# Performance work log

Measured on AMD Instinct MI355X. Metric: run time of the kernel, lower is better.

## Reference

```python
import jax, jax.numpy as jnp
import numpy as np

N_NODES = 100000


def gcn_conv(x, edge_index, W, b, n_nodes):
    """PyG GCNConv: add self-loops, symmetric deg norm, linear, scatter-add, bias."""
    self_loops = jnp.arange(n_nodes, dtype=edge_index.dtype)
    src = jnp.concatenate([edge_index[0], self_loops])  # [E+N]
    dst = jnp.concatenate([edge_index[1], self_loops])  # [E+N]
    xw = x @ W  # [N, out]
    deg = jax.ops.segment_sum(jnp.ones_like(dst, dtype=xw.dtype), dst, num_segments=n_nodes)
    deg_inv_sqrt = jnp.where(deg > 0, jax.lax.rsqrt(deg), 0.0)
    norm = deg_inv_sqrt[src] * deg_inv_sqrt[dst]  # [E+N]
    msg = xw[src] * norm[:, None]                 # [E+N, out]
    out = jax.ops.segment_sum(msg, dst, num_segments=n_nodes)
    return out + b


def setup_inputs() -> dict:
    key = jax.random.key(0)
    ks = jax.random.split(key, 8)
    n, e, d_in, h = N_NODES, 3200000, 128, 16
    x = jax.random.normal(ks[0], (n, d_in), dtype=jnp.float32)
    edge_index = jax.random.randint(ks[1], (2, e), 0, n, dtype=jnp.int64)
    W1 = jax.random.normal(ks[2], (d_in, h), dtype=jnp.float32) / np.sqrt(d_in)
    b1 = jnp.zeros((h,), dtype=jnp.float32)
    W2 = jax.random.normal(ks[3], (h, h), dtype=jnp.float32) / np.sqrt(h)
    b2 = jnp.zeros((h,), dtype=jnp.float32)
    W_lin = jax.random.normal(ks[4], (h, 1), dtype=jnp.float32) / np.sqrt(h)
    b_lin = jnp.zeros((1,), dtype=jnp.float32)
    return {"x": x, "edge_index": edge_index, "W1": W1, "b1": b1,
            "W2": W2, "b2": b2, "W_lin": W_lin, "b_lin": b_lin}


def reference(x, edge_index, W1, b1, W2, b2, W_lin, b_lin):
    n = x.shape[0]
    h = gcn_conv(x, edge_index, W1, b1, n)
    h = jax.nn.relu(h)
    # dropout is identity in eval mode (training=False)
    h = gcn_conv(h, edge_index, W2, b2, n)
    h = jax.nn.relu(h)
    out = h @ W_lin + b_lin  # [N, 1]
    return out.squeeze(-1)   # [N]
```

## Files before the change

### kernel.cpp

```cpp
#include <hip/hip_runtime.h>
#include <hip/hip_fp16.h>

#define DIN 128
#define HDIM 16
#define NB 256
#define CAP 13312
#define CAPC 14848
#define CAPH (CAPC / 2)
#define BIN_EPT 16
#define BINSZ (256 * BIN_EPT)

__device__ __forceinline__ float4 f4add(float4 a, float4 b) {
    return make_float4(a.x + b.x, a.y + b.y, a.z + b.z, a.w + b.w);
}

__device__ __forceinline__ float4 h4_to_f4(uint2 u) {
    __half2 a = *(__half2*)&u.x, b = *(__half2*)&u.y;
    float2 fa = __half22float2(a), fb = __half22float2(b);
    return make_float4(fa.x, fa.y, fb.x, fb.y);
}
__device__ __forceinline__ uint2 f4_to_h4(float4 v) {
    __half2 a = __floats2half2_rn(v.x, v.y);
    __half2 b = __floats2half2_rn(v.z, v.w);
    uint2 u;
    u.x = *(unsigned*)&a;
    u.y = *(unsigned*)&b;
    return u;
}

__device__ __forceinline__ int load_idx(const void* ei, long long i, int is64) {
    return is64 ? (int)((const long long*)ei)[i] : ((const int*)ei)[i];
}

__global__ __launch_bounds__(256) void k_main(const void* __restrict__ ei, long long E,
                                              int bdiv, unsigned Mdiv,
                                              int* __restrict__ bcur,
                                              unsigned int* __restrict__ recs,
                                              const float* __restrict__ x,
                                              const float* __restrict__ W1,
                                              unsigned int* __restrict__ y1,
                                              int n, int nbin) {
    __shared__ int cnt[NB];
    __shared__ int base[NB];
    __shared__ float Ws[DIN * HDIM];
    int tid = threadIdx.x;
    if ((int)blockIdx.x < nbin) {
        unsigned probe = ((const unsigned*)ei)[1 + 2 * (tid & 63)];
        int is64 = (__ballot(probe != 0) == 0ull) ? 1 : 0;
        if (tid < NB) cnt[tid] = 0;
        __syncthreads();
        long long e0 = (long long)blockIdx.x * BINSZ;
        int s[BIN_EPT], dl[BIN_EPT], b[BIN_EPT];
#pragma unroll
        for (int i = 0; i < BIN_EPT; i++) {
            long long e = e0 + (long long)i * 256 + tid;
            if (e < E) {
                s[i] = load_idx(ei, e, is64);
                int d = load_idx(ei, E + e, is64);
                int bb = Mdiv ? (int)__umulhi((unsigned)d, Mdiv) : d;
                b[i] = bb;
                dl[i] = d - bb * bdiv;
                atomicAdd(&cnt[bb], 1);
            } else {
                b[i] = -1;
            }
        }
        __syncthreads();
        if (tid < NB) {
            base[tid] = atomicAdd(&bcur[tid], cnt[tid]);
            cnt[tid] = 0;
        }
        __syncthreads();
#pragma unroll
        for (int i = 0; i < BIN_EPT; i++) {
            if (b[i] >= 0) {
                int off = atomicAdd(&cnt[b[i]], 1);
                int pos = base[b[i]] + off;
                if (pos < CAP) {
                    recs[(size_t)b[i] * CAP + pos] =
                        ((unsigned)dl[i] << 18) | (unsigned)s[i];
                }
            }
        }
    } else {
        for (int i = tid; i < DIN * HDIM; i += 256) Ws[i] = W1[i];
        __syncthreads();
        int node = ((int)blockIdx.x - nbin) * 256 + tid;
        if (node > n) return;
        uint2* yr = (uint2*)(y1 + (size_t)node * 8);
        if (node == n) {
            uint2 z; z.x = 0u; z.y = 0u;
#pragma unroll
            for (int q = 0; q < 4; q++) yr[q] = z;
            return;
        }
        float acc[HDIM];
#pragma unroll
        for (int f = 0; f < HDIM; f++) acc[f] = 0.f;
        const float4* xr = (const float4*)(x + (size_t)node * DIN);
#pragma unroll 8
        for (int k4 = 0; k4 < DIN / 4; k4++) {
            float4 xv = xr[k4];
            int k = k4 * 4;
#pragma unroll
            for (int f = 0; f < HDIM; f++) {
                acc[f] += xv.x * Ws[(k + 0) * HDIM + f];
                acc[f] += xv.y * Ws[(k + 1) * HDIM + f];
                acc[f] += xv.z * Ws[(k + 2) * HDIM + f];
                acc[f] += xv.w * Ws[(k + 3) * HDIM + f];
            }
        }
#pragma unroll
        for (int q = 0; q < 4; q++)
            yr[q] = f4_to_h4(make_float4(acc[q * 4 + 0], acc[q * 4 + 1],
                                         acc[q * 4 + 2], acc[q * 4 + 3]));
    }
}

__global__ __launch_bounds__(512) void k_prep(const unsigned int* __restrict__ recs,
                                              const int* __restrict__ bcur,
                                              float* __restrict__ dis,
                                              unsigned int* __restrict__ meta,
                                              int* __restrict__ col,
                                              unsigned int* __restrict__ y1,
                                              int bdiv, int n) {
    __shared__ int cnt_sh[256];
    __shared__ int sc[256];
    __shared__ unsigned short buf[CAPH];
    int tid = threadIdx.x;
    int b = (int)blockIdx.x >> 1;
    int h = (int)blockIdx.x & 1;
    int hd = (bdiv + 1) >> 1;
    int lo_f = b * bdiv; if (lo_f > n) lo_f = n;
    int hi_f = lo_f + bdiv; if (hi_f > n) hi_f = n;
    int lo = lo_f + h * hd; if (lo > hi_f) lo = hi_f;
    int hi = lo + hd; if (hi > hi_f) hi = hi_f;
    int nd = hi - lo;
    int dbase = h * hd;
    if (tid < 256) cnt_sh[tid] = 0;
    __syncthreads();
    int m = bcur[b]; if (m > CAP) m = CAP;
    const unsigned int* r = recs + (size_t)b * CAP;
    for (int i = tid; i < m; i += 512) {
        int j = (int)(r[i] >> 18) - dbase;
        if ((unsigned)j < (unsigned)nd) atomicAdd(&cnt_sh[j], 1);
    }
    __syncthreads();
    int v  = (tid < nd) ? cnt_sh[tid] : 0;
    int pv = (v + 3) & ~3;
    if (tid < 256) sc[tid] = pv;
    __syncthreads();
    for (int off = 1; off < 256; off <<= 1) {
        int t = (tid >= off && tid < 256) ? sc[tid - off] : 0;
        __syncthreads();
        if (tid < 256) sc[tid] += t;
        __syncthreads();
    }
    int ptot = sc[255];
    if (ptot > CAPH) ptot = CAPH;
    int cbase = b * CAPC + h * CAPH;
    if (tid < nd) {
        int excl = sc[tid] - pv;
        dis[lo + tid] = rsqrtf((float)v + 1.0f);
        meta[lo + tid] = ((unsigned)(cbase + excl) << 10) | (unsigned)v;
        cnt_sh[tid] = excl;
    }
    for (int i = tid; i < ptot; i += 512) buf[i] = 0xFFFFu;
    __syncthreads();
    for (int i = tid; i < m; i += 512) {
        int j = (int)(r[i] >> 18) - dbase;
        if ((unsigned)j < (unsigned)nd) {
            int pos = atomicAdd(&cnt_sh[j], 1);
            if (pos < CAPH) buf[pos] = (unsigned short)i;
        }
    }
    __syncthreads();
    for (int i = tid; i < ptot; i += 512) {
        unsigned short bi = buf[i];
        col[cbase + i] = (bi == 0xFFFFu) ? n : (int)(r[bi] & 0x3FFFFu);
    }
    int q = tid & 3, slot = tid >> 2;
    uint2* yv = (uint2*)y1;
    for (int j = slot; j < nd; j += 128) {
        int node = lo + j;
        float dv = dis[node];
        float4 t = h4_to_f4(yv[(size_t)node * 4 + q]);
        yv[(size_t)node * 4 + q] =
            f4_to_h4(make_float4(t.x * dv, t.y * dv, t.z * dv, t.w * dv));
    }
}

__global__ __launch_bounds__(256) void k_gather1(const unsigned int* __restrict__ meta,
                                                 const int* __restrict__ col,
                                                 const unsigned int* __restrict__ y1,
                                                 const float* __restrict__ dis,
                                                 const float* __restrict__ b1,
                                                 const float* __restrict__ W2,
                                                 unsigned int* __restrict__ y2, int n) {
    __shared__ float4 Ws4[HDIM][4];
    if (threadIdx.x < HDIM * 4)
        ((float4*)Ws4)[threadIdx.x] = ((const float4*)W2)[threadIdx.x];
    __syncthreads();
    if (blockIdx.x == 0 && threadIdx.x < 4) {
        uint2 z; z.x = 0u; z.y = 0u;
        ((uint2*)y2)[(size_t)n * 4 + threadIdx.x] = z;
    }
    int ln = threadIdx.x >> 2;
    int q  = threadIdx.x & 3;
    int node = blockIdx.x * 64 + ln;
    if (node >= n) return;
    unsigned mt = meta[node];
    int start = (int)(mt >> 10);
    int endp  = start + (((int)(mt & 1023u) + 3) & ~3);
    const uint2* yv = (const uint2*)y1;
    float4 a0 = make_float4(0.f, 0.f, 0.f, 0.f), a1 = a0, a2 = a0, a3 = a0;
    int e = start;
    for (; e + 16 <= endp; e += 16) {
        int4 c4 = *(const int4*)(col + e + 4 * q);
        int s[16];
#pragma unroll
        for (int j = 0; j < 4; j++) {
            s[4 * j + 0] = __shfl(c4.x, j, 4);
            s[4 * j + 1] = __shfl(c4.y, j, 4);
            s[4 * j + 2] = __shfl(c4.z, j, 4);
            s[4 * j + 3] = __shfl(c4.w, j, 4);
        }
        uint2 v[16];
#pragma unroll
        for (int k = 0; k < 16; k++) v[k] = yv[(size_t)s[k] * 4 + q];
#pragma unroll
        for (int k = 0; k < 16; k += 4) {
            a0 = f4add(a0, h4_to_f4(v[k + 0]));
            a1 = f4add(a1, h4_to_f4(v[k + 1]));
            a2 = f4add(a2, h4_to_f4(v[k + 2]));
            a3 = f4add(a3, h4_to_f4(v[k + 3]));
        }
    }
    for (; e < endp; e += 4) {
        int4 c4 = *(const int4*)(col + e);
        uint2 v0 = yv[(size_t)c4.x * 4 + q];
        uint2 v1 = yv[(size_t)c4.y * 4 + q];
        uint2 v2 = yv[(size_t)c4.z * 4 + q];
        uint2 v3 = yv[(size_t)c4.w * 4 + q];
        a0 = f4add(a0, h4_to_f4(v0)); a1 = f4add(a1, h4_to_f4(v1));
        a2 = f4add(a2, h4_to_f4(v2)); a3 = f4add(a3, h4_to_f4(v3));
    }
    float4 acc = f4add(f4add(a0, a1), f4add(a2, a3));
    acc = f4add(acc, h4_to_f4(yv[(size_t)node * 4 + q]));
    float dv = dis[node];
    float4 bb = ((const float4*)b1)[q];
    float4 h;
    h.x = fmaxf(dv * acc.x + bb.x, 0.f);
    h.y = fmaxf(dv * acc.y + bb.y, 0.f);
    h.z = fmaxf(dv * acc.z + bb.z, 0.f);
    h.w = fmaxf(dv * acc.w + bb.w, 0.f);
    float4 o = make_float4(0.f, 0.f, 0.f, 0.f);
#pragma unroll
    for (int k = 0; k < 4; k++) {
        float4 hk;
        hk.x = __shfl(h.x, k, 4); hk.y = __shfl(h.y, k, 4);
        hk.z = __shfl(h.z, k, 4); hk.w = __shfl(h.w, k, 4);
        float hv[4] = {hk.x, hk.y, hk.z, hk.w};
#pragma unroll
        for (int c = 0; c < 4; c++) {
            float4 w = Ws4[k * 4 + c][q];
            o.x += hv[c] * w.x; o.y += hv[c] * w.y;
            o.z += hv[c] * w.z; o.w += hv[c] * w.w;
        }
    }
    ((uint2*)y2)[(size_t)node * 4 + q] =
        f4_to_h4(make_float4(o.x * dv, o.y * dv, o.z * dv, o.w * dv));
}

__global__ __launch_bounds__(256) void k_gather2(const unsigned int* __restrict__ meta,
                                                 const int* __restrict__ col,
                                                 const unsigned int* __restrict__ y2,
                                                 const float* __restrict__ dis,
                                                 const float* __restrict__ b2,
                                                 const float* __restrict__ Wlin,
                                                 const float* __restrict__ blin,
                                                 float* __restrict__ out, int n) {
    int ln = threadIdx.x >> 2;
    int q  = threadIdx.x & 3;
    int node = blockIdx.x * 64 + ln;
    if (node >= n) return;
    unsigned mt = meta[node];
    int start = (int)(mt >> 10);
    int endp  = start + (((int)(mt & 1023u) + 3) & ~3);
    const uint2* yv = (const uint2*)y2;
    float4 a0 = make_float4(0.f, 0.f, 0.f, 0.f), a1 = a0, a2 = a0, a3 = a0;
    int e = start;
    for (; e + 16 <= endp; e += 16) {
        int4 c4 = *(const int4*)(col + e + 4 * q);
        int s[16];
#pragma unroll
        for (int j = 0; j < 4; j++) {
            s[4 * j + 0] = __shfl(c4.x, j, 4);
            s[4 * j + 1] = __shfl(c4.y, j, 4);
            s[4 * j + 2] = __shfl(c4.z, j, 4);
            s[4 * j + 3] = __shfl(c4.w, j, 4);
        }
        uint2 v[16];
#pragma unroll
        for (int k = 0; k < 16; k++) v[k] = yv[(size_t)s[k] * 4 + q];
#pragma unroll
        for (int k = 0; k < 16; k += 4) {
            a0 = f4add(a0, h4_to_f4(v[k + 0]));
            a1 = f4add(a1, h4_to_f4(v[k + 1]));
            a2 = f4add(a2, h4_to_f4(v[k + 2]));
            a3 = f4add(a3, h4_to_f4(v[k + 3]));
        }
    }
    for (; e < endp; e += 4) {
        int4 c4 = *(const int4*)(col + e);
        uint2 v0 = yv[(size_t)c4.x * 4 + q];
        uint2 v1 = yv[(size_t)c4.y * 4 + q];
        uint2 v2 = yv[(size_t)c4.z * 4 + q];
        uint2 v3 = yv[(size_t)c4.w * 4 + q];
        a0 = f4add(a0, h4_to_f4(v0)); a1 = f4add(a1, h4_to_f4(v1));
        a2 = f4add(a2, h4_to_f4(v2)); a3 = f4add(a3, h4_to_f4(v3));
    }
    float4 acc = f4add(f4add(a0, a1), f4add(a2, a3));
    acc = f4add(acc, h4_to_f4(yv[(size_t)node * 4 + q]));
    float dv = dis[node];
    float4 bb = ((const float4*)b2)[q];
    float4 wl = ((const float4*)Wlin)[q];
    float v = 0.f;
    v += fmaxf(dv * acc.x + bb.x, 0.f) * wl.x;
    v += fmaxf(dv * acc.y + bb.y, 0.f) * wl.y;
    v += fmaxf(dv * acc.z + bb.z, 0.f) * wl.z;
    v += fmaxf(dv * acc.w + bb.w, 0.f) * wl.w;
    v += __shfl_xor(v, 1, 4);
    v += __shfl_xor(v, 2, 4);
    if (q == 0) out[node] = v + blin[0];
}

extern "C" void kernel_launch(void* const* d_in, const int* in_sizes, int n_in,
                              void* d_out, int out_size, void* d_ws, size_t ws_size,
                              hipStream_t stream) {
    const float* x    = (const float*)d_in[0];
    const void*  ei   = d_in[1];
    const float* W1   = (const float*)d_in[2];
    const float* b1   = (const float*)d_in[3];
    const float* W2   = (const float*)d_in[4];
    const float* b2   = (const float*)d_in[5];
    const float* Wlin = (const float*)d_in[6];
    const float* blin = (const float*)d_in[7];
    float* out = (float*)d_out;

    const int n = in_sizes[0] / DIN;
    const long long E = in_sizes[1] / 2;
    const int bdiv = (n + NB - 1) / NB;
    const unsigned Mdiv = (bdiv > 1)
        ? (unsigned)(((1ull << 32) + (unsigned)bdiv - 1) / (unsigned)bdiv) : 0u;

    char* ws = (char*)d_ws;
    size_t off = 0;
    auto alloc = [&](size_t bytes) { char* p = ws + off; off += (bytes + 255) & ~(size_t)255; return p; };
    int*   bcur   = (int*)alloc(NB * 4);
    float* dis    = (float*)alloc((size_t)n * 4);
    unsigned int* meta = (unsigned int*)alloc((size_t)n * 4);
    unsigned int* y1   = (unsigned int*)alloc((size_t)(n + 1) * 8 * 4);
    size_t region_elems = (size_t)NB * CAP;
    if (region_elems < (size_t)(n + 1) * 8) region_elems = (size_t)(n + 1) * 8;
    char*  region = alloc(region_elems * 4);
    unsigned int* recs = (unsigned int*)region;
    unsigned int* y2   = (unsigned int*)region;
    int*   col    = (int*)alloc((size_t)NB * CAPC * 4);

    const int nb_xw  = (n + 1 + 255) / 256;
    const int nb_bin = (int)((E + BINSZ - 1) / BINSZ);
    const int nb_g   = (n + 63) / 64;

    hipMemsetAsync(bcur, 0, NB * sizeof(int), stream);
    k_main<<<nb_bin + nb_xw, 256, 0, stream>>>(ei, E, bdiv, Mdiv, bcur, recs, x, W1, y1, n, nb_bin);
    k_prep<<<2 * NB, 512, 0, stream>>>(recs, bcur, dis, meta, col, y1, bdiv, n);
    k_gather1<<<nb_g, 256, 0, stream>>>(meta, col, y1, dis, b1, W2, y2, n);
    k_gather2<<<nb_g, 256, 0, stream>>>(meta, col, y2, dis, b2, Wlin, blin, out, n);
}
```

Before: 217.4 us.

## Replace CSR build with per-bin shared-memory atomic aggregation over binned edges

Drops the CSR construction kernel (the col/meta arrays and the padded sentinel row). The two aggregation layers now read the binned edge records directly: each of 512 bins, covering about 196 destination nodes, accumulates neighbor features into a shared-memory tile with float atomics, then applies bias, ReLU and the small matmul. Degrees come from a lightweight counting kernel, and the bin count doubles while per-bin capacity shrinks. This removes a full scatter/sort pass and its memory traffic. In exchange, each layer issues many LDS atomics, keeps fewer loads in flight per thread, and runs only 512 large blocks, which may hurt latency hiding for the random gathers.

```diff
diff --git a/kernel.cpp b/kernel.cpp
--- a/kernel.cpp
+++ b/kernel.cpp
@@ -3,10 +3,10 @@
 
 #define DIN 128
 #define HDIM 16
-#define NB 256
-#define CAP 13312
-#define CAPC 14848
-#define CAPH (CAPC / 2)
+#define NB 512
+#define BDIV_MAX 256
+#define CAPB 7168
+#define HSTR 17
 #define BIN_EPT 16
 #define BINSZ (256 * BIN_EPT)
 
@@ -47,7 +47,7 @@
     if ((int)blockIdx.x < nbin) {
         unsigned probe = ((const unsigned*)ei)[1 + 2 * (tid & 63)];
         int is64 = (__ballot(probe != 0) == 0ull) ? 1 : 0;
-        if (tid < NB) cnt[tid] = 0;
+        cnt[tid] = 0; cnt[tid + 256] = 0;
         __syncthreads();
         long long e0 = (long long)blockIdx.x * BINSZ;
         int s[BIN_EPT], dl[BIN_EPT], b[BIN_EPT];
@@ -66,9 +66,11 @@
             }
         }
         __syncthreads();
-        if (tid < NB) {
-            base[tid] = atomicAdd(&bcur[tid], cnt[tid]);
-            cnt[tid] = 0;
+        {
+            int t = tid;
+            base[t] = atomicAdd(&bcur[t], cnt[t]); cnt[t] = 0;
+            t = tid + 256;
+            base[t] = atomicAdd(&bcur[t], cnt[t]); cnt[t] = 0;
         }
         __syncthreads();
 #pragma unroll
@@ -76,8 +78,8 @@
             if (b[i] >= 0) {
                 int off = atomicAdd(&cnt[b[i]], 1);
                 int pos = base[b[i]] + off;
-                if (pos < CAP) {
-                    recs[(size_t)b[i] * CAP + pos] =
+                if (pos < CAPB) {
+                    recs[(size_t)b[i] * CAPB + pos] =
                         ((unsigned)dl[i] << 18) | (unsigned)s[i];
                 }
             }
@@ -86,14 +88,8 @@
         for (int i = tid; i < DIN * HDIM; i += 256) Ws[i] = W1[i];
         __syncthreads();
         int node = ((int)blockIdx.x - nbin) * 256 + tid;
-        if (node > n) return;
+        if (node >= n) return;
         uint2* yr = (uint2*)(y1 + (size_t)node * 8);
-        if (node == n) {
-            uint2 z; z.x = 0u; z.y = 0u;
-#pragma unroll
-            for (int q = 0; q < 4; q++) yr[q] = z;
-            return;
-        }
         float acc[HDIM];
 #pragma unroll
         for (int f = 0; f < HDIM; f++) acc[f] = 0.f;
@@ -117,222 +113,165 @@
     }
 }
 
-__global__ __launch_bounds__(512) void k_prep(const unsigned int* __restrict__ recs,
-                                              const int* __restrict__ bcur,
-                                              float* __restrict__ dis,
-                                              unsigned int* __restrict__ meta,
-                                              int* __restrict__ col,
-                                              unsigned int* __restrict__ y1,
-                                              int bdiv, int n) {
-    __shared__ int cnt_sh[256];
-    __shared__ int sc[256];
-    __shared__ unsigned short buf[CAPH];
-    int tid = threadIdx.x;
-    int b = (int)blockIdx.x >> 1;
-    int h = (int)blockIdx.x & 1;
-    int hd = (bdiv + 1) >> 1;
-    int lo_f = b * bdiv; if (lo_f > n) lo_f = n;
-    int hi_f = lo_f + bdiv; if (hi_f > n) hi_f = n;
-    int lo = lo_f + h * hd; if (lo > hi_f) lo = hi_f;
-    int hi = lo + hd; if (hi > hi_f) hi = hi_f;
+__global__ __launch_bounds__(512) void k_deg(const unsigned int* __restrict__ recs,
+                                             const int* __restrict__ bcur,
+                                             float* __restrict__ dis,
+                                             unsigned int* __restrict__ y1,
+                                             int n, int bdiv) {
+    __shared__ int cnt[BDIV_MAX];
+    int tid = threadIdx.x, b = blockIdx.x;
+    if (tid < BDIV_MAX) cnt[tid] = 0;
+    __syncthreads();
+    int lo = b * bdiv; if (lo > n) lo = n;
+    int hi = lo + bdiv; if (hi > n) hi = n;
     int nd = hi - lo;
-    int dbase = h * hd;
-    if (tid < 256) cnt_sh[tid] = 0;
-    __syncthreads();
-    int m = bcur[b]; if (m > CAP) m = CAP;
-    const unsigned int* r = recs + (size_t)b * CAP;
-    for (int i = tid; i < m; i += 512) {
-        int j = (int)(r[i] >> 18) - dbase;
-        if ((unsigned)j < (unsigned)nd) atomicAdd(&cnt_sh[j], 1);
-    }
-    __syncthreads();
-    int v  = (tid < nd) ? cnt_sh[tid] : 0;
-    int pv = (v + 3) & ~3;
-    if (tid < 256) sc[tid] = pv;
-    __syncthreads();
-    for (int off = 1; off < 256; off <<= 1) {
-        int t = (tid >= off && tid < 256) ? sc[tid - off] : 0;
-        __syncthreads();
-        if (tid < 256) sc[tid] += t;
-        __syncthreads();
-    }
-    int ptot = sc[255];
-    if (ptot > CAPH) ptot = CAPH;
-    int cbase = b * CAPC + h * CAPH;
-    if (tid < nd) {
-        int excl = sc[tid] - pv;
-        dis[lo + tid] = rsqrtf((float)v + 1.0f);
-        meta[lo + tid] = ((unsigned)(cbase + excl) << 10) | (unsigned)v;
-        cnt_sh[tid] = excl;
-    }
-    for (int i = tid; i < ptot; i += 512) buf[i] = 0xFFFFu;
-    __syncthreads();
-    for (int i = tid; i < m; i += 512) {
-        int j = (int)(r[i] >> 18) - dbase;
-        if ((unsigned)j < (unsigned)nd) {
-            int pos = atomicAdd(&cnt_sh[j], 1);
-            if (pos < CAPH) buf[pos] = (unsigned short)i;
-        }
-    }
-    __syncthreads();
-    for (int i = tid; i < ptot; i += 512) {
-        unsigned short bi = buf[i];
-        col[cbase + i] = (bi == 0xFFFFu) ? n : (int)(r[bi] & 0x3FFFFu);
-    }
-    int q = tid & 3, slot = tid >> 2;
+    int m = bcur[b]; if (m > CAPB) m = CAPB;
+    const unsigned int* r = recs + (size_t)b * CAPB;
+    for (int i = tid; i < m; i += 512)
+        atomicAdd(&cnt[r[i] >> 18], 1);
+    __syncthreads();
+    int q = tid & 3, g = tid >> 2;
     uint2* yv = (uint2*)y1;
-    for (int j = slot; j < nd; j += 128) {
+    for (int j = g; j < nd; j += 128) {
         int node = lo + j;
-        float dv = dis[node];
+        float dv = rsqrtf((float)cnt[j] + 1.0f);
+        if (q == 0) dis[node] = dv;
         float4 t = h4_to_f4(yv[(size_t)node * 4 + q]);
         yv[(size_t)node * 4 + q] =
             f4_to_h4(make_float4(t.x * dv, t.y * dv, t.z * dv, t.w * dv));
     }
 }
 
-__global__ __launch_bounds__(256) void k_gather1(const unsigned int* __restrict__ meta,
-                                                 const int* __restrict__ col,
-                                                 const unsigned int* __restrict__ y1,
-                                                 const float* __restrict__ dis,
-                                                 const float* __restrict__ b1,
-                                                 const float* __restrict__ W2,
-                                                 unsigned int* __restrict__ y2, int n) {
+__global__ __launch_bounds__(512) void k_agg1(const unsigned int* __restrict__ recs,
+                                              const int* __restrict__ bcur,
+                                              const float* __restrict__ dis,
+                                              const unsigned int* __restrict__ y1,
+                                              const float* __restrict__ b1,
+                                              const float* __restrict__ W2,
+                                              unsigned int* __restrict__ y2,
+                                              int n, int bdiv) {
+    __shared__ float acc[BDIV_MAX * HSTR];
     __shared__ float4 Ws4[HDIM][4];
-    if (threadIdx.x < HDIM * 4)
-        ((float4*)Ws4)[threadIdx.x] = ((const float4*)W2)[threadIdx.x];
-    __syncthreads();
-    if (blockIdx.x == 0 && threadIdx.x < 4) {
-        uint2 z; z.x = 0u; z.y = 0u;
-        ((uint2*)y2)[(size_t)n * 4 + threadIdx.x] = z;
-    }
-    int ln = threadIdx.x >> 2;
-    int q  = threadIdx.x & 3;
-    int node = blockIdx.x * 64 + ln;
-    if (node >= n) return;
-    unsigned mt = meta[node];
-    int start = (int)(mt >> 10);
-    int endp  = start + (((int)(mt & 1023u) + 3) & ~3);
+    int tid = threadIdx.x, b = blockIdx.x;
+    if (tid < HDIM * 4)
+        ((float4*)Ws4)[tid] = ((const float4*)W2)[tid];
+    int lo = b * bdiv; if (lo > n) lo = n;
+    int hi = lo + bdiv; if (hi > n) hi = n;
+    int nd = hi - lo;
+    for (int i = tid; i < bdiv * HSTR; i += 512) acc[i] = 0.f;
+    __syncthreads();
+    int m = bcur[b]; if (m > CAPB) m = CAPB;
+    const unsigned int* r = recs + (size_t)b * CAPB;
     const uint2* yv = (const uint2*)y1;
-    float4 a0 = make_float4(0.f, 0.f, 0.f, 0.f), a1 = a0, a2 = a0, a3 = a0;
-    int e = start;
-    for (; e + 16 <= endp; e += 16) {
-        int4 c4 = *(const int4*)(col + e + 4 * q);
-        int s[16];
-#pragma unroll
-        for (int j = 0; j < 4; j++) {
-            s[4 * j + 0] = __shfl(c4.x, j, 4);
-            s[4 * j + 1] = __shfl(c4.y, j, 4);
-            s[4 * j + 2] = __shfl(c4.z, j, 4);
-            s[4 * j + 3] = __shfl(c4.w, j, 4);
-        }
-        uint2 v[16];
-#pragma unroll
-        for (int k = 0; k < 16; k++) v[k] = yv[(size_t)s[k] * 4 + q];
-#pragma unroll
-        for (int k = 0; k < 16; k += 4) {
-            a0 = f4add(a0, h4_to_f4(v[k + 0]));
-            a1 = f4add(a1, h4_to_f4(v[k + 1]));
-            a2 = f4add(a2, h4_to_f4(v[k + 2]));
-            a3 = f4add(a3, h4_to_f4(v[k + 3]));
-        }
-    }
-    for (; e < endp; e += 4) {
-        int4 c4 = *(const int4*)(col + e);
-        uint2 v0 = yv[(size_t)c4.x * 4 + q];
-        uint2 v1 = yv[(size_t)c4.y * 4 + q];
-        uint2 v2 = yv[(size_t)c4.z * 4 + q];
-        uint2 v3 = yv[(size_t)c4.w * 4 + q];
-        a0 = f4add(a0, h4_to_f4(v0)); a1 = f4add(a1, h4_to_f4(v1));
-        a2 = f4add(a2, h4_to_f4(v2)); a3 = f4add(a3, h4_to_f4(v3));
-    }
-    float4 acc = f4add(f4add(a0, a1), f4add(a2, a3));
-    acc = f4add(acc, h4_to_f4(yv[(size_t)node * 4 + q]));
-    float dv = dis[node];
+    int q = tid & 3, g = tid >> 2;
+    int i = g;
+    for (; i + 128 < m; i += 256) {
+        unsigned r0 = r[i], r1 = r[i + 128];
+        float4 v0 = h4_to_f4(yv[(size_t)(r0 & 0x3FFFFu) * 4 + q]);
+        float4 v1 = h4_to_f4(yv[(size_t)(r1 & 0x3FFFFu) * 4 + q]);
+        float* a0 = &acc[(r0 >> 18) * HSTR + q * 4];
+        float* a1 = &acc[(r1 >> 18) * HSTR + q * 4];
+        atomicAdd(a0 + 0, v0.x); atomicAdd(a0 + 1, v0.y);
+        atomicAdd(a0 + 2, v0.z); atomicAdd(a0 + 3, v0.w);
+        atomicAdd(a1 + 0, v1.x); atomicAdd(a1 + 1, v1.y);
+        atomicAdd(a1 + 2, v1.z); atomicAdd(a1 + 3, v1.w);
+    }
+    if (i < m) {
+        unsigned r0 = r[i];
+        float4 v0 = h4_to_f4(yv[(size_t)(r0 & 0x3FFFFu) * 4 + q]);
+        float* a0 = &acc[(r0 >> 18) * HSTR + q * 4];
+        atomicAdd(a0 + 0, v0.x); atomicAdd(a0 + 1, v0.y);
+        atomicAdd(a0 + 2, v0.z); atomicAdd(a0 + 3, v0.w);
+    }
+    __syncthreads();
     float4 bb = ((const float4*)b1)[q];
-    float4 h;
-    h.x = fmaxf(dv * acc.x + bb.x, 0.f);
-    h.y = fmaxf(dv * acc.y + bb.y, 0.f);
-    h.z = fmaxf(dv * acc.z + bb.z, 0.f);
-    h.w = fmaxf(dv * acc.w + bb.w, 0.f);
-    float4 o = make_float4(0.f, 0.f, 0.f, 0.f);
-#pragma unroll
-    for (int k = 0; k < 4; k++) {
-        float4 hk;
-        hk.x = __shfl(h.x, k, 4); hk.y = __shfl(h.y, k, 4);
-        hk.z = __shfl(h.z, k, 4); hk.w = __shfl(h.w, k, 4);
-        float hv[4] = {hk.x, hk.y, hk.z, hk.w};
-#pragma unroll
-        for (int c = 0; c < 4; c++) {
-            float4 w = Ws4[k * 4 + c][q];
-            o.x += hv[c] * w.x; o.y += hv[c] * w.y;
-            o.z += hv[c] * w.z; o.w += hv[c] * w.w;
-        }
-    }
-    ((uint2*)y2)[(size_t)node * 4 + q] =
-        f4_to_h4(make_float4(o.x * dv, o.y * dv, o.z * dv, o.w * dv));
-}
-
-__global__ __launch_bounds__(256) void k_gather2(const unsigned int* __restrict__ meta,
-                                                 const int* __restrict__ col,
-                                                 const unsigned int* __restrict__ y2,
-                                                 const float* __restrict__ dis,
-                                                 const float* __restrict__ b2,
-                                                 const float* __restrict__ Wlin,
-                                                 const float* __restrict__ blin,
-                                                 float* __restrict__ out, int n) {
-    int ln = threadIdx.x >> 2;
-    int q  = threadIdx.x & 3;
-    int node = blockIdx.x * 64 + ln;
-    if (node >= n) return;
-    unsigned mt = meta[node];
-    int start = (int)(mt >> 10);
-    int endp  = start + (((int)(mt & 1023u) + 3) & ~3);
+    for (int j = g; j < nd; j += 128) {
+        int node = lo + j;
+        float dv = dis[node];
+        float* ap = &acc[j * HSTR + q * 4];
+        float4 a = make_float4(ap[0], ap[1], ap[2], ap[3]);
+        a = f4add(a, h4_to_f4(yv[(size_t)node * 4 + q]));
+        float4 h;
+        h.x = fmaxf(dv * a.x + bb.x, 0.f);
+        h.y = fmaxf(dv * a.y + bb.y, 0.f);
+        h.z = fmaxf(dv * a.z + bb.z, 0.f);
+        h.w = fmaxf(dv * a.w + bb.w, 0.f);
+        float4 o = make_float4(0.f, 0.f, 0.f, 0.f);
+#pragma unroll
+        for (int k = 0; k < 4; k++) {
+            float4 hk;
+            hk.x = __shfl(h.x, k, 4); hk.y = __shfl(h.y, k, 4);
+            hk.z = __shfl(h.z, k, 4); hk.w = __shfl(h.w, k, 4);
+            float hv[4] = {hk.x, hk.y, hk.z, hk.w};
+#pragma unroll
+            for (int c = 0; c < 4; c++) {
+                float4 w = Ws4[k * 4 + c][q];
+                o.x += hv[c] * w.x; o.y += hv[c] * w.y;
+                o.z += hv[c] * w.z; o.w += hv[c] * w.w;
+            }
+        }
+        ((uint2*)y2)[(size_t)node * 4 + q] =
+            f4_to_h4(make_float4(o.x * dv, o.y * dv, o.z * dv, o.w * dv));
+    }
+}
+
+__global__ __launch_bounds__(512) void k_agg2(const unsigned int* __restrict__ recs,
+                                              const int* __restrict__ bcur,
+                                              const float* __restrict__ dis,
+                                              const unsigned int* __restrict__ y2,
+                                              const float* __restrict__ b2,
+                                              const float* __restrict__ Wlin,
+                                              const float* __restrict__ blin,
+                                              float* __restrict__ out,
+                                              int n, int bdiv) {
+    __shared__ float acc[BDIV_MAX * HSTR];
+    int tid = threadIdx.x, b = blockIdx.x;
+    int lo = b * bdiv; if (lo > n) lo = n;
+    int hi = lo + bdiv; if (hi > n) hi = n;
+    int nd = hi - lo;
+    for (int i = tid; i < bdiv * HSTR; i += 512) acc[i] = 0.f;
+    __syncthreads();
+    int m = bcur[b]; if (m > CAPB) m = CAPB;
+    const unsigned int* r = recs + (size_t)b * CAPB;
     const uint2* yv = (const uint2*)y2;
-    float4 a0 = make_float4(0.f, 0.f, 0.f, 0.f), a1 = a0, a2 = a0, a3 = a0;
-    int e = start;
-    for (; e + 16 <= endp; e += 16) {
-        int4 c4 = *(const int4*)(col + e + 4 * q);
-        int s[16];
-#pragma unroll
-        for (int j = 0; j < 4; j++) {
-            s[4 * j + 0] = __shfl(c4.x, j, 4);
-            s[4 * j + 1] = __shfl(c4.y, j, 4);
-            s[4 * j + 2] = __shfl(c4.z, j, 4);
-            s[4 * j + 3] = __shfl(c4.w, j, 4);
-        }
-        uint2 v[16];
-#pragma unroll
-        for (int k = 0; k < 16; k++) v[k] = yv[(size_t)s[k] * 4 + q];
-#pragma unroll
-        for (int k = 0; k < 16; k += 4) {
-            a0 = f4add(a0, h4_to_f4(v[k + 0]));
-            a1 = f4add(a1, h4_to_f4(v[k + 1]));
-            a2 = f4add(a2, h4_to_f4(v[k + 2]));
-            a3 = f4add(a3, h4_to_f4(v[k + 3]));
-        }
-    }
-    for (; e < endp; e += 4) {
-        int4 c4 = *(const int4*)(col + e);
-        uint2 v0 = yv[(size_t)c4.x * 4 + q];
-        uint2 v1 = yv[(size_t)c4.y * 4 + q];
-        uint2 v2 = yv[(size_t)c4.z * 4 + q];
-        uint2 v3 = yv[(size_t)c4.w * 4 + q];
-        a0 = f4add(a0, h4_to_f4(v0)); a1 = f4add(a1, h4_to_f4(v1));
-        a2 = f4add(a2, h4_to_f4(v2)); a3 = f4add(a3, h4_to_f4(v3));
-    }
-    float4 acc = f4add(f4add(a0, a1), f4add(a2, a3));
-    acc = f4add(acc, h4_to_f4(yv[(size_t)node * 4 + q]));
-    float dv = dis[node];
+    int q = tid & 3, g = tid >> 2;
+    int i = g;
+    for (; i + 128 < m; i += 256) {
+        unsigned r0 = r[i], r1 = r[i + 128];
+        float4 v0 = h4_to_f4(yv[(size_t)(r0 & 0x3FFFFu) * 4 + q]);
+        float4 v1 = h4_to_f4(yv[(size_t)(r1 & 0x3FFFFu) * 4 + q]);
+        float* a0 = &acc[(r0 >> 18) * HSTR + q * 4];
+        float* a1 = &acc[(r1 >> 18) * HSTR + q * 4];
+        atomicAdd(a0 + 0, v0.x); atomicAdd(a0 + 1, v0.y);
+        atomicAdd(a0 + 2, v0.z); atomicAdd(a0 + 3, v0.w);
+        atomicAdd(a1 + 0, v1.x); atomicAdd(a1 + 1, v1.y);
+        atomicAdd(a1 + 2, v1.z); atomicAdd(a1 + 3, v1.w);
+    }
+    if (i < m) {
+        unsigned r0 = r[i];
+        float4 v0 = h4_to_f4(yv[(size_t)(r0 & 0x3FFFFu) * 4 + q]);
+        float* a0 = &acc[(r0 >> 18) * HSTR + q * 4];
+        atomicAdd(a0 + 0, v0.x); atomicAdd(a0 + 1, v0.y);
+        atomicAdd(a0 + 2, v0.z); atomicAdd(a0 + 3, v0.w);
+    }
+    __syncthreads();
     float4 bb = ((const float4*)b2)[q];
     float4 wl = ((const float4*)Wlin)[q];
-    float v = 0.f;
-    v += fmaxf(dv * acc.x + bb.x, 0.f) * wl.x;
-    v += fmaxf(dv * acc.y + bb.y, 0.f) * wl.y;
-    v += fmaxf(dv * acc.z + bb.z, 0.f) * wl.z;
-    v += fmaxf(dv * acc.w + bb.w, 0.f) * wl.w;
-    v += __shfl_xor(v, 1, 4);
-    v += __shfl_xor(v, 2, 4);
-    if (q == 0) out[node] = v + blin[0];
+    for (int j = g; j < nd; j += 128) {
+        int node = lo + j;
+        float dv = dis[node];
+        float* ap = &acc[j * HSTR + q * 4];
+        float4 a = make_float4(ap[0], ap[1], ap[2], ap[3]);
+        a = f4add(a, h4_to_f4(yv[(size_t)node * 4 + q]));
+        float v = 0.f;
+        v += fmaxf(dv * a.x + bb.x, 0.f) * wl.x;
+        v += fmaxf(dv * a.y + bb.y, 0.f) * wl.y;
+        v += fmaxf(dv * a.z + bb.z, 0.f) * wl.z;
+        v += fmaxf(dv * a.w + bb.w, 0.f) * wl.w;
+        v += __shfl_xor(v, 1, 4);
+        v += __shfl_xor(v, 2, 4);
+        if (q == 0) out[node] = v + blin[0];
+    }
 }
 
 extern "C" void kernel_launch(void* const* d_in, const int* in_sizes, int n_in,
@@ -357,24 +296,18 @@
     char* ws = (char*)d_ws;
     size_t off = 0;
     auto alloc = [&](size_t bytes) { char* p = ws + off; off += (bytes + 255) & ~(size_t)255; return p; };
-    int*   bcur   = (int*)alloc(NB * 4);
-    float* dis    = (float*)alloc((size_t)n * 4);
-    unsigned int* meta = (unsigned int*)alloc((size_t)n * 4);
-    unsigned int* y1   = (unsigned int*)alloc((size_t)(n + 1) * 8 * 4);
-    size_t region_elems = (size_t)NB * CAP;
-    if (region_elems < (size_t)(n + 1) * 8) region_elems = (size_t)(n + 1) * 8;
-    char*  region = alloc(region_elems * 4);
-    unsigned int* recs = (unsigned int*)region;
-    unsigned int* y2   = (unsigned int*)region;
-    int*   col    = (int*)alloc((size_t)NB * CAPC * 4);
-
-    const int nb_xw  = (n + 1 + 255) / 256;
+    int*   bcur = (int*)alloc(NB * 4);
+    float* dis  = (float*)alloc((size_t)n * 4);
+    unsigned int* y1 = (unsigned int*)alloc((size_t)n * 8 * 4);
+    unsigned int* y2 = (unsigned int*)alloc((size_t)n * 8 * 4);
+    unsigned int* recs = (unsigned int*)alloc((size_t)NB * CAPB * 4);
+
+    const int nb_xw  = (n + 255) / 256;
     const int nb_bin = (int)((E + BINSZ - 1) / BINSZ);
-    const int nb_g   = (n + 63) / 64;
 
     hipMemsetAsync(bcur, 0, NB * sizeof(int), stream);
     k_main<<<nb_bin + nb_xw, 256, 0, stream>>>(ei, E, bdiv, Mdiv, bcur, recs, x, W1, y1, n, nb_bin);
-    k_prep<<<2 * NB, 512, 0, stream>>>(recs, bcur, dis, meta, col, y1, bdiv, n);
-    k_gather1<<<nb_g, 256, 0, stream>>>(meta, col, y1, dis, b1, W2, y2, n);
-    k_gather2<<<nb_g, 256, 0, stream>>>(meta, col, y2, dis, b2, Wlin, blin, out, n);
-}
+    k_deg<<<NB, 512, 0, stream>>>(recs, bcur, dis, y1, n, bdiv);
+    k_agg1<<<NB, 512, 0, stream>>>(recs, bcur, dis, y1, b1, W2, y2, n, bdiv);
+    k_agg2<<<NB, 512, 0, stream>>>(recs, bcur, dis, y2, b2, Wlin, blin, out, n, bdiv);
+}
```

New measurement: 673.8 us. +209.9%, slower.
